# Kernel optimization log

Hardware: AMD Instinct MI355X
Metric: run time of the kernel (lower is better)

The kernel has to match this reference:

```python
import jax, jax.numpy as jnp
import numpy as np

V = 6890   # SMPL vertices
K = 24     # joints
NB = 10    # shape betas
NP = 207   # pose blendshape basis = 23*9
PARENTS = np.array([-1, 0, 0, 0, 1, 2, 3, 4, 5, 6, 7, 8, 9, 9, 9, 12, 13, 14, 16, 17, 18, 19, 20, 21])


def setup_inputs() -> dict:
    key = jax.random.key(0)
    ks = jax.random.split(key, 8)
    B = 1024
    body_pose = jax.random.normal(ks[0], (B, 69), dtype=jnp.float32) * 0.2
    betas = jax.random.normal(ks[1], (B, NB), dtype=jnp.float32)
    global_orient = jax.random.normal(ks[2], (B, 3), dtype=jnp.float32) * 0.2
    v_template = jax.random.normal(ks[3], (V, 3), dtype=jnp.float32) * 0.1
    shapedirs = jax.random.normal(ks[4], (V, 3, NB), dtype=jnp.float32) * 0.01
    posedirs = jax.random.normal(ks[5], (NP, V * 3), dtype=jnp.float32) * 0.01
    J_regressor = jax.nn.softmax(jax.random.normal(ks[6], (K, V), dtype=jnp.float32), axis=-1)
    lbs_weights = jax.nn.softmax(jax.random.normal(ks[7], (V, K), dtype=jnp.float32) * 4.0, axis=-1)
    parents = jnp.asarray(PARENTS, dtype=jnp.int32)
    return dict(body_pose=body_pose, betas=betas, global_orient=global_orient,
                v_template=v_template, shapedirs=shapedirs, posedirs=posedirs,
                J_regressor=J_regressor, lbs_weights=lbs_weights, parents=parents)


def _rodrigues(aa):
    # aa: [..., 3] axis-angle -> [..., 3, 3] rotation matrices
    angle = jnp.linalg.norm(aa + 1e-8, axis=-1, keepdims=True)  # [...,1]
    axis = aa / angle
    sin = jnp.sin(angle)[..., None]
    cos = jnp.cos(angle)[..., None]
    rx, ry, rz = axis[..., 0], axis[..., 1], axis[..., 2]
    z = jnp.zeros_like(rx)
    Km = jnp.stack([z, -rz, ry, rz, z, -rx, -ry, rx, z], axis=-1).reshape(aa.shape[:-1] + (3, 3))
    ident = jnp.eye(3, dtype=aa.dtype)
    return ident + sin * Km + (1.0 - cos) * (Km @ Km)


def reference(body_pose, betas, global_orient, v_template, shapedirs, posedirs,
              J_regressor, lbs_weights, parents):
    full_pose = jnp.concatenate([global_orient, body_pose], axis=1)  # [B,72]
    B = betas.shape[0]
    dtype = betas.dtype

    # shape blend shapes
    v_shaped = v_template + jnp.einsum('bl,vkl->bvk', betas, shapedirs)  # [B,V,3]
    # rest joints
    joints_t = jnp.einsum('jv,bvk->bjk', J_regressor, v_shaped)          # [B,K,3]

    # pose -> rotation matrices (pose2rot=True path)
    rot_mats = _rodrigues(full_pose.reshape(B, K, 3))                    # [B,K,3,3]

    # pose blend shapes
    ident = jnp.eye(3, dtype=dtype)
    pose_feature = (rot_mats[:, 1:] - ident).reshape(B, NP)              # [B,207]
    v_posed = v_shaped + (pose_feature @ posedirs).reshape(B, V, 3)

    # kinematic chain (batch_rigid_transform)
    rel_joints = joints_t.at[:, 1:].add(-joints_t[:, PARENTS[1:]])       # [B,K,3]
    tm = jnp.concatenate([rot_mats, rel_joints[..., None]], axis=-1)     # [B,K,3,4]
    bottom = jnp.broadcast_to(jnp.array([0., 0., 0., 1.], dtype=dtype), (B, K, 1, 4))
    tm = jnp.concatenate([tm, bottom], axis=-2)                          # [B,K,4,4]
    chain = [tm[:, 0]]
    for i in range(1, K):  # fixed small kinematic tree
        chain.append(chain[PARENTS[i]] @ tm[:, i])
    transforms = jnp.stack(chain, axis=1)                                # [B,K,4,4]
    joints = transforms[..., :3, 3]                                      # posed joints

    # relative transforms: subtract rotated rest-joint position
    A = transforms.at[..., :3, 3].add(
        -jnp.einsum('bkij,bkj->bki', transforms[..., :3, :3], joints_t))  # [B,K,4,4]

    # linear blend skinning
    T = jnp.einsum('vk,bkij->bvij', lbs_weights, A)                      # [B,V,4,4]
    vertices = jnp.einsum('bvij,bvj->bvi', T[..., :3, :3], v_posed) + T[..., :3, 3]
    return vertices, joints_t, joints, rot_mats
```

## Files before the change

### kernel.cpp

```cpp
#include <hip/hip_runtime.h>
#include <hip/hip_bf16.h>

#define VNUM 6890
#define KJ 24
#define NBETA 10
#define NPOSE 207
#define KPAD 224
#define BATCH 1024
#define N3 20670
#define NVG 431
#define NROWF 20688

#define OUT_V  0
#define OUT_JT 21166080
#define OUT_J  21239808
#define OUT_RM 21313536

#define WS_JVJS 0
#define WS_ABFF 792
#define WS_WBFF 262936
#define WS_PFBF 373528
#define WS_PDTF 488216

typedef unsigned short ushort;
typedef __attribute__((ext_vector_type(8))) short short8v;
typedef __attribute__((ext_vector_type(4))) float floatx4;

__device__ __forceinline__ ushort f2bfu(float x) {
  __hip_bfloat16 h = __float2bfloat16(x);
  union { __hip_bfloat16 h; ushort u; } cv; cv.h = h; return cv.u;
}

__global__ __launch_bounds__(256) void jreg_kernel(
    const float* __restrict__ Jr, const float* __restrict__ vt,
    const float* __restrict__ sd, float* __restrict__ JvJs) {
  const int j = blockIdx.x;
  const int chunk = blockIdx.y;
  const int t = threadIdx.x;
  const int lane = t & 63, wid = t >> 6;
  const int vbeg = chunk * 1723;
  const int vend = (vbeg + 1723 < VNUM) ? vbeg + 1723 : VNUM;
  __shared__ float red[4][33];
  float acc[33];
#pragma unroll
  for (int q = 0; q < 33; q++) acc[q] = 0.0f;
  for (int v = vbeg + t; v < vend; v += 256) {
    float r = Jr[j * VNUM + v];
    const float* vtp = vt + v * 3;
    const float* sdp = sd + v * 30;
    acc[0] += r * vtp[0];
    acc[1] += r * vtp[1];
    acc[2] += r * vtp[2];
#pragma unroll
    for (int q = 0; q < 30; q++) acc[3 + q] += r * sdp[q];
  }
#pragma unroll
  for (int q = 0; q < 33; q++) {
    float x = acc[q];
    for (int off = 32; off > 0; off >>= 1) x += __shfl_down(x, off, 64);
    if (lane == 0) red[wid][q] = x;
  }
  __syncthreads();
  if (t < 33)
    atomicAdd(&JvJs[j * 33 + t], red[0][t] + red[1][t] + red[2][t] + red[3][t]);
}

__global__ __launch_bounds__(64) void batch_prep(
    const float* __restrict__ body_pose, const float* __restrict__ betas,
    const float* __restrict__ global_orient, const float* __restrict__ JvJs,
    float* __restrict__ out_jt, float* __restrict__ out_j, float* __restrict__ out_rm,
    ushort* __restrict__ pfbf, ushort* __restrict__ Abff) {
  const int b = blockIdx.x;
  const int t = threadIdx.x;
  __shared__ float R[24][9];
  __shared__ float jt[24][3];
  __shared__ float chR[24][9];
  __shared__ float cht[24][3];

  if (t < 24) {
    float ax, ay, az;
    if (t == 0) {
      ax = global_orient[b * 3 + 0];
      ay = global_orient[b * 3 + 1];
      az = global_orient[b * 3 + 2];
    } else {
      const float* p = body_pose + (size_t)b * 69 + (t - 1) * 3;
      ax = p[0]; ay = p[1]; az = p[2];
    }
    float px = ax + 1e-8f, py = ay + 1e-8f, pz = az + 1e-8f;
    float angle = sqrtf(px * px + py * py + pz * pz);
    float inv = 1.0f / angle;
    float rx = ax * inv, ry = ay * inv, rz = az * inv;
    float s = sinf(angle), c = cosf(angle);
    float cc = 1.0f - c;
    float m[9];
    m[0] = 1.0f - cc * (ry * ry + rz * rz);
    m[1] = -s * rz + cc * rx * ry;
    m[2] =  s * ry + cc * rx * rz;
    m[3] =  s * rz + cc * rx * ry;
    m[4] = 1.0f - cc * (rx * rx + rz * rz);
    m[5] = -s * rx + cc * ry * rz;
    m[6] = -s * ry + cc * rx * rz;
    m[7] =  s * rx + cc * ry * rz;
    m[8] = 1.0f - cc * (rx * rx + ry * ry);
#pragma unroll
    for (int e = 0; e < 9; e++) {
      R[t][e] = m[e];
      out_rm[(size_t)b * 216 + t * 9 + e] = m[e];
    }
  }
  for (int idx = t; idx < 72; idx += 64) {
    int j = idx / 3, c = idx % 3;
    const float* JJ = JvJs + j * 33;
    float s = JJ[c];
    const float* be = betas + (size_t)b * NBETA;
#pragma unroll
    for (int l = 0; l < NBETA; l++) s += be[l] * JJ[3 + c * 10 + l];
    jt[j][c] = s;
    out_jt[(size_t)b * 72 + idx] = s;
  }
  __syncthreads();
  for (int mI = t; mI < KPAD; mI += 64) {
    float val = 0.0f;
    if (mI < NPOSE) {
      int k = 1 + mI / 9, e = mI % 9;
      val = R[k][e] - ((e == 0 || e == 4 || e == 8) ? 1.0f : 0.0f);
    } else if (mI < NPOSE + NBETA) {
      val = betas[(size_t)b * NBETA + (mI - NPOSE)];
    }
    int kb = mI >> 5, quad = (mI >> 3) & 3, j = mI & 7;
    pfbf[(size_t)(((b >> 4) * 7 + kb) * 512) + (quad * 16 + (b & 15)) * 8 + j] =
        f2bfu(val);
  }
  if (t == 0) {
    const int par[24] = {-1, 0, 0, 0, 1, 2, 3, 4, 5, 6, 7, 8, 9, 9, 9, 12, 13, 14, 16, 17, 18, 19, 20, 21};
#pragma unroll
    for (int e = 0; e < 9; e++) chR[0][e] = R[0][e];
    cht[0][0] = jt[0][0]; cht[0][1] = jt[0][1]; cht[0][2] = jt[0][2];
    for (int k = 1; k < 24; k++) {
      int p = par[k];
      float rel0 = jt[k][0] - jt[p][0];
      float rel1 = jt[k][1] - jt[p][1];
      float rel2 = jt[k][2] - jt[p][2];
#pragma unroll
      for (int i = 0; i < 3; i++) {
        float a0 = chR[p][i * 3 + 0], a1 = chR[p][i * 3 + 1], a2 = chR[p][i * 3 + 2];
        chR[k][i * 3 + 0] = a0 * R[k][0] + a1 * R[k][3] + a2 * R[k][6];
        chR[k][i * 3 + 1] = a0 * R[k][1] + a1 * R[k][4] + a2 * R[k][7];
        chR[k][i * 3 + 2] = a0 * R[k][2] + a1 * R[k][5] + a2 * R[k][8];
        cht[k][i] = a0 * rel0 + a1 * rel1 + a2 * rel2 + cht[p][i];
      }
    }
  }
  __syncthreads();
  if (t < 24) {
    int k = t;
#pragma unroll
    for (int i = 0; i < 3; i++) out_j[(size_t)b * 72 + k * 3 + i] = cht[k][i];
  }
  for (int e = t; e < 512; e += 64) {
    int quad = e >> 7, n = (e >> 3) & 15, j = e & 7;
    int k = quad * 8 + j;
    float val = 0.0f;
    if (n < 12 && k < 24) {
      int i = n >> 2, jj = n & 3;
      if (jj < 3) {
        val = chR[k][i * 3 + jj];
      } else {
        val = cht[k][i] - (chR[k][i * 3 + 0] * jt[k][0] +
                           chR[k][i * 3 + 1] * jt[k][1] +
                           chR[k][i * 3 + 2] * jt[k][2]);
      }
    }
    Abff[(size_t)b * 512 + e] = f2bfu(val);
  }
}

__global__ __launch_bounds__(256) void transpose_pd(
    const float* __restrict__ pd, ushort* __restrict__ pdTf,
    const float* __restrict__ sd,
    const float* __restrict__ w, ushort* __restrict__ wbff) {
  {
    int lb = blockIdx.y * 324 + blockIdx.x;
    if (lb < 864) {
      int i = lb * 256 + threadIdx.x;
      int vg = i >> 9, e = i & 511;
      int quad = e >> 7, l15 = (e >> 3) & 15, j = e & 7;
      int v = vg * 16 + l15, k = quad * 8 + j;
      float x = (v < VNUM && k < 24) ? w[v * 24 + k] : 0.0f;
      wbff[i] = f2bfu(x);
    }
  }
  __shared__ float tile[32][65];
  const int t = threadIdx.x;
  const int n0 = blockIdx.x * 64;
  const int k0 = blockIdx.y * 32;
  const int c = t & 63;
  for (int r = t >> 6; r < 32; r += 4) {
    int k = k0 + r, n = n0 + c;
    float x = 0.0f;
    if (n < N3) {
      if (k < NPOSE) x = pd[(size_t)k * N3 + n];
      else if (k < NPOSE + NBETA) x = sd[(size_t)n * 10 + (k - NPOSE)];
    }
    tile[r][c] = x;
  }
  __syncthreads();
  const int n = t >> 2;
  const int j0 = (t & 3) * 8;
  const int rg = n0 + n;
  if (rg >= NROWF) return;
  unsigned int outw[4];
#pragma unroll
  for (int jj = 0; jj < 4; jj++) {
    unsigned int lo = f2bfu(tile[j0 + jj * 2][n]);
    unsigned int hi = f2bfu(tile[j0 + jj * 2 + 1][n]);
    outw[jj] = lo | (hi << 16);
  }
  const int vg = rg / 48;
  const int rl = rg - vg * 48;
  const int ns = rl >> 4, l15 = rl & 15;
  const int kb = k0 >> 5, quad = j0 >> 3;
  *(uint4*)&pdTf[(size_t)(((vg * 3 + ns) * 7 + kb) * 512) + (quad * 16 + l15) * 8] =
      make_uint4(outw[0], outw[1], outw[2], outw[3]);
}

__global__ __launch_bounds__(128, 6) void fused_mfma(
    const ushort* __restrict__ pfbf, const ushort* __restrict__ pdTf,
    const float* __restrict__ vt, const ushort* __restrict__ wbff,
    const ushort* __restrict__ Abff, float* __restrict__ out_v) {
  __shared__ float vpS[32 * 50];
  const int tid = threadIdx.x;
  const int lane = tid & 63, wv = tid >> 6;
  const int l15 = lane & 15, quad = lane >> 4;

  const int bid = blockIdx.x;
  const int L = (bid & 7) * 1724 + (bid >> 3);
  const int bm = (L & 31) * 32 + wv * 16;
  const int vg = L >> 5;

  const short8v wf = *(const short8v*)(wbff + (size_t)vg * 512 + lane * 8);
  const int gn0 = vg * 48 + l15;
  float vt0 = (gn0      < N3) ? vt[gn0]      : 0.0f;
  float vt1 = (gn0 + 16 < N3) ? vt[gn0 + 16] : 0.0f;
  float vt2 = (gn0 + 32 < N3) ? vt[gn0 + 32] : 0.0f;

  const ushort* apf = pfbf + (size_t)((bm >> 4) * 7) * 512 + lane * 8;
  const ushort* bpf = pdTf + (size_t)(vg * 21) * 512 + lane * 8;

  floatx4 acc0 = {0.0f, 0.0f, 0.0f, 0.0f};
  floatx4 acc1 = acc0, acc2 = acc0;
#pragma unroll
  for (int kb = 0; kb < 7; kb++) {
    short8v a  = *(const short8v*)(apf + kb * 512);
    short8v b0 = *(const short8v*)(bpf + (0 * 7 + kb) * 512);
    short8v b1 = *(const short8v*)(bpf + (1 * 7 + kb) * 512);
    short8v b2 = *(const short8v*)(bpf + (2 * 7 + kb) * 512);
    acc0 = __builtin_amdgcn_mfma_f32_16x16x32_bf16(a, b0, acc0, 0, 0, 0);
    acc1 = __builtin_amdgcn_mfma_f32_16x16x32_bf16(a, b1, acc1, 0, 0, 0);
    acc2 = __builtin_amdgcn_mfma_f32_16x16x32_bf16(a, b2, acc2, 0, 0, 0);
  }

  float* myvp = &vpS[wv * 16 * 50];
#pragma unroll
  for (int r = 0; r < 4; r++) {
    int row = quad * 4 + r;
    myvp[row * 50 +      l15] = acc0[r] + vt0;
    myvp[row * 50 + 16 + l15] = acc1[r] + vt1;
    myvp[row * 50 + 32 + l15] = acc2[r] + vt2;
  }
  __builtin_amdgcn_sched_barrier(0);
  __builtin_amdgcn_s_waitcnt(0xc07f);
  __builtin_amdgcn_sched_barrier(0);

  const int gv = vg * 16 + l15;
  const bool active = (quad < 3) && (gv < VNUM);
  const ushort* abase = Abff + (size_t)bm * 512 + lane * 8;
  float* outp = out_v + (size_t)bm * N3 + (size_t)gv * 3 + quad;
  const float* pbase = myvp + 3 * l15;

  short8v apre[4];
  float ppx[4], ppy[4], ppz[4];
#pragma unroll
  for (int i = 0; i < 4; i++) {
    apre[i] = *(const short8v*)(abase + i * 512);
    ppx[i] = pbase[i * 50 + 0];
    ppy[i] = pbase[i * 50 + 1];
    ppz[i] = pbase[i * 50 + 2];
  }

  const floatx4 zero = {0.0f, 0.0f, 0.0f, 0.0f};
#pragma unroll
  for (int i = 0; i < 16; i++) {
    const int slot = i & 3;
    short8v afrag = apre[slot];
    float px = ppx[slot], py = ppy[slot], pz = ppz[slot];
    if (i < 12) {
      apre[slot] = *(const short8v*)(abase + (i + 4) * 512);
      ppx[slot] = pbase[(i + 4) * 50 + 0];
      ppy[slot] = pbase[(i + 4) * 50 + 1];
      ppz[slot] = pbase[(i + 4) * 50 + 2];
    }
    floatx4 t = zero;
    t = __builtin_amdgcn_mfma_f32_16x16x32_bf16(afrag, wf, t, 0, 0, 0);
    if (active) {
      *outp = t[0] * px + t[1] * py + t[2] * pz + t[3];
    }
    outp += N3;
  }
}

extern "C" void kernel_launch(void* const* d_in, const int* in_sizes, int n_in,
                              void* d_out, int out_size, void* d_ws, size_t ws_size,
                              hipStream_t stream) {
  const float* body_pose     = (const float*)d_in[0];
  const float* betas         = (const float*)d_in[1];
  const float* global_orient = (const float*)d_in[2];
  const float* v_template    = (const float*)d_in[3];
  const float* shapedirs     = (const float*)d_in[4];
  const float* posedirs      = (const float*)d_in[5];
  const float* J_regressor   = (const float*)d_in[6];
  const float* lbs_weights   = (const float*)d_in[7];

  float* out = (float*)d_out;
  float* out_v  = out + OUT_V;
  float* out_jt = out + OUT_JT;
  float* out_j  = out + OUT_J;
  float* out_rm = out + OUT_RM;

  float* ws = (float*)d_ws;
  float* JvJs = ws + WS_JVJS;
  ushort* Abff = (ushort*)(ws + WS_ABFF);
  ushort* wbff = (ushort*)(ws + WS_WBFF);
  ushort* pfbf = (ushort*)(ws + WS_PFBF);
  ushort* pdTf = (ushort*)(ws + WS_PDTF);

  hipMemsetAsync(JvJs, 0, KJ * 33 * sizeof(float), stream);
  jreg_kernel<<<dim3(KJ, 4), 256, 0, stream>>>(J_regressor, v_template, shapedirs, JvJs);
  transpose_pd<<<dim3(324, 7), 256, 0, stream>>>(posedirs, pdTf, shapedirs,
                                                 lbs_weights, wbff);
  batch_prep<<<BATCH, 64, 0, stream>>>(body_pose, betas, global_orient, JvJs,
                                       out_jt, out_j, out_rm, pfbf, Abff);
  fused_mfma<<<13792, 128, 0, stream>>>(pfbf, pdTf, v_template, wbff, Abff, out_v);
}
```

Measured before the change: 198.3 us.

## Retile fused MFMA kernel: 4 vertex groups per block sharing A in LDS

Each block now uses 4 waves covering 4 vertex groups and 32 batch rows, with each wave doing both 16-row batch halves of the pose GEMM. The per-batch skinning transform fragments are loaded cooperatively once per block into shared memory and reused by all four vertex-group waves, rather than each wave streaming them from global memory. This cuts redundant global reads of the A transforms and of pdTf, at the cost of a block-wide barrier, more LDS per block, lower occupancy and a few clamped idle waves at the tail.

```diff
diff --git a/kernel.cpp b/kernel.cpp
--- a/kernel.cpp
+++ b/kernel.cpp
@@ -225,84 +225,94 @@
       make_uint4(outw[0], outw[1], outw[2], outw[3]);
 }
 
-__global__ __launch_bounds__(128, 6) void fused_mfma(
+__global__ __launch_bounds__(256, 2) void fused_mfma(
     const ushort* __restrict__ pfbf, const ushort* __restrict__ pdTf,
     const float* __restrict__ vt, const ushort* __restrict__ wbff,
     const ushort* __restrict__ Abff, float* __restrict__ out_v) {
-  __shared__ float vpS[32 * 50];
+  __shared__ __align__(16) ushort AbS[32 * 512];
+  __shared__ float vpS[4][32 * 50];
   const int tid = threadIdx.x;
   const int lane = tid & 63, wv = tid >> 6;
   const int l15 = lane & 15, quad = lane >> 4;
 
   const int bid = blockIdx.x;
-  const int L = (bid & 7) * 1724 + (bid >> 3);
-  const int bm = (L & 31) * 32 + wv * 16;
-  const int vg = L >> 5;
-
-  const short8v wf = *(const short8v*)(wbff + (size_t)vg * 512 + lane * 8);
-  const int gn0 = vg * 48 + l15;
+  const int L = (bid & 7) * 432 + (bid >> 3);
+  const int bt = L & 31;
+  const int q  = L >> 5;
+  const int bm = bt * 32;
+  const int vg = q * 4 + wv;
+  const int vgc = (vg < NVG) ? vg : (NVG - 1);
+
+  short8v ab[8];
+  {
+    const ushort* asrc = Abff + (size_t)(bm + wv * 8) * 512 + lane * 8;
+#pragma unroll
+    for (int j = 0; j < 8; j++) ab[j] = *(const short8v*)(asrc + j * 512);
+  }
+
+  const short8v wf = *(const short8v*)(wbff + (size_t)vgc * 512 + lane * 8);
+  const int gn0 = vgc * 48 + l15;
   float vt0 = (gn0      < N3) ? vt[gn0]      : 0.0f;
   float vt1 = (gn0 + 16 < N3) ? vt[gn0 + 16] : 0.0f;
   float vt2 = (gn0 + 32 < N3) ? vt[gn0 + 32] : 0.0f;
 
-  const ushort* apf = pfbf + (size_t)((bm >> 4) * 7) * 512 + lane * 8;
-  const ushort* bpf = pdTf + (size_t)(vg * 21) * 512 + lane * 8;
-
-  floatx4 acc0 = {0.0f, 0.0f, 0.0f, 0.0f};
-  floatx4 acc1 = acc0, acc2 = acc0;
+  const ushort* apf0 = pfbf + (size_t)((bm >> 4) * 7) * 512 + lane * 8;
+  const ushort* apf1 = apf0 + 7 * 512;
+  const ushort* bpf  = pdTf + (size_t)(vgc * 21) * 512 + lane * 8;
+
+  const floatx4 zero = {0.0f, 0.0f, 0.0f, 0.0f};
+  floatx4 acc[2][3];
+#pragma unroll
+  for (int bg = 0; bg < 2; bg++)
+#pragma unroll
+    for (int ns = 0; ns < 3; ns++) acc[bg][ns] = zero;
+
 #pragma unroll
   for (int kb = 0; kb < 7; kb++) {
-    short8v a  = *(const short8v*)(apf + kb * 512);
+    short8v a0 = *(const short8v*)(apf0 + kb * 512);
+    short8v a1 = *(const short8v*)(apf1 + kb * 512);
     short8v b0 = *(const short8v*)(bpf + (0 * 7 + kb) * 512);
     short8v b1 = *(const short8v*)(bpf + (1 * 7 + kb) * 512);
     short8v b2 = *(const short8v*)(bpf + (2 * 7 + kb) * 512);
-    acc0 = __builtin_amdgcn_mfma_f32_16x16x32_bf16(a, b0, acc0, 0, 0, 0);
-    acc1 = __builtin_amdgcn_mfma_f32_16x16x32_bf16(a, b1, acc1, 0, 0, 0);
-    acc2 = __builtin_amdgcn_mfma_f32_16x16x32_bf16(a, b2, acc2, 0, 0, 0);
-  }
-
-  float* myvp = &vpS[wv * 16 * 50];
-#pragma unroll
-  for (int r = 0; r < 4; r++) {
-    int row = quad * 4 + r;
-    myvp[row * 50 +      l15] = acc0[r] + vt0;
-    myvp[row * 50 + 16 + l15] = acc1[r] + vt1;
-    myvp[row * 50 + 32 + l15] = acc2[r] + vt2;
-  }
-  __builtin_amdgcn_sched_barrier(0);
-  __builtin_amdgcn_s_waitcnt(0xc07f);
-  __builtin_amdgcn_sched_barrier(0);
-
-  const int gv = vg * 16 + l15;
-  const bool active = (quad < 3) && (gv < VNUM);
-  const ushort* abase = Abff + (size_t)bm * 512 + lane * 8;
+    acc[0][0] = __builtin_amdgcn_mfma_f32_16x16x32_bf16(a0, b0, acc[0][0], 0, 0, 0);
+    acc[0][1] = __builtin_amdgcn_mfma_f32_16x16x32_bf16(a0, b1, acc[0][1], 0, 0, 0);
+    acc[0][2] = __builtin_amdgcn_mfma_f32_16x16x32_bf16(a0, b2, acc[0][2], 0, 0, 0);
+    acc[1][0] = __builtin_amdgcn_mfma_f32_16x16x32_bf16(a1, b0, acc[1][0], 0, 0, 0);
+    acc[1][1] = __builtin_amdgcn_mfma_f32_16x16x32_bf16(a1, b1, acc[1][1], 0, 0, 0);
+    acc[1][2] = __builtin_amdgcn_mfma_f32_16x16x32_bf16(a1, b2, acc[1][2], 0, 0, 0);
+  }
+
+  float* myvp = vpS[wv];
+#pragma unroll
+  for (int bg = 0; bg < 2; bg++) {
+#pragma unroll
+    for (int r = 0; r < 4; r++) {
+      int row = bg * 16 + quad * 4 + r;
+      myvp[row * 50 +      l15] = acc[bg][0][r] + vt0;
+      myvp[row * 50 + 16 + l15] = acc[bg][1][r] + vt1;
+      myvp[row * 50 + 32 + l15] = acc[bg][2][r] + vt2;
+    }
+  }
+
+  {
+    ushort* adst = AbS + (size_t)(wv * 8) * 512 + lane * 8;
+#pragma unroll
+    for (int j = 0; j < 8; j++) *(short8v*)(adst + j * 512) = ab[j];
+  }
+  __syncthreads();
+
+  const int gv = vgc * 16 + l15;
+  const bool active = (quad < 3) && (vg < NVG) && (gv < VNUM);
   float* outp = out_v + (size_t)bm * N3 + (size_t)gv * 3 + quad;
   const float* pbase = myvp + 3 * l15;
 
-  short8v apre[4];
-  float ppx[4], ppy[4], ppz[4];
-#pragma unroll
-  for (int i = 0; i < 4; i++) {
-    apre[i] = *(const short8v*)(abase + i * 512);
-    ppx[i] = pbase[i * 50 + 0];
-    ppy[i] = pbase[i * 50 + 1];
-    ppz[i] = pbase[i * 50 + 2];
-  }
-
-  const floatx4 zero = {0.0f, 0.0f, 0.0f, 0.0f};
-#pragma unroll
-  for (int i = 0; i < 16; i++) {
-    const int slot = i & 3;
-    short8v afrag = apre[slot];
-    float px = ppx[slot], py = ppy[slot], pz = ppz[slot];
-    if (i < 12) {
-      apre[slot] = *(const short8v*)(abase + (i + 4) * 512);
-      ppx[slot] = pbase[(i + 4) * 50 + 0];
-      ppy[slot] = pbase[(i + 4) * 50 + 1];
-      ppz[slot] = pbase[(i + 4) * 50 + 2];
-    }
-    floatx4 t = zero;
-    t = __builtin_amdgcn_mfma_f32_16x16x32_bf16(afrag, wf, t, 0, 0, 0);
+#pragma unroll
+  for (int i = 0; i < 32; i++) {
+    short8v afrag = *(const short8v*)&AbS[i * 512 + lane * 8];
+    floatx4 t = __builtin_amdgcn_mfma_f32_16x16x32_bf16(afrag, wf, zero, 0, 0, 0);
+    float px = pbase[i * 50 + 0];
+    float py = pbase[i * 50 + 1];
+    float pz = pbase[i * 50 + 2];
     if (active) {
       *outp = t[0] * px + t[1] * py + t[2] * pz + t[3];
     }
@@ -341,5 +351,5 @@
                                                  lbs_weights, wbff);
   batch_prep<<<BATCH, 64, 0, stream>>>(body_pose, betas, global_orient, JvJs,
                                        out_jt, out_j, out_rm, pfbf, Abff);
-  fused_mfma<<<13792, 128, 0, stream>>>(pfbf, pdTf, v_template, wbff, Abff, out_v);
-}
+  fused_mfma<<<3456, 256, 0, stream>>>(pfbf, pdTf, v_template, wbff, Abff, out_v);
+}
```

Result: no change. 197.1 us (-0.6%).
